# Kernel tuning notes

Measured on AMD Instinct MI355X. Metric: run time of the kernel, lower is better.

The kernel has to match this reference:

```python
import jax, jax.numpy as jnp
import numpy as np

DIM = 512
HEADS = 8


def setup_inputs() -> dict:
    key = jax.random.key(0)
    k1, k2, k3 = jax.random.split(key, 3)
    x = jax.random.normal(k1, (4, DIM, 64, 64), dtype=jnp.float32)
    # kaiming_normal fan_out, linear: std = 1/sqrt(fan_out)
    w_qkv = jax.random.normal(k2, (3 * DIM, DIM), dtype=jnp.float32) / np.sqrt(3 * DIM)
    b_qkv = jnp.zeros((3 * DIM,), dtype=jnp.float32)
    w_proj = jax.random.normal(k3, (DIM, DIM), dtype=jnp.float32) / np.sqrt(DIM)
    b_proj = jnp.zeros((DIM,), dtype=jnp.float32)
    return {"x": x, "w_qkv": w_qkv, "b_qkv": b_qkv, "w_proj": w_proj, "b_proj": b_proj}


def reference(x, w_qkv, b_qkv, w_proj, b_proj):
    B, C, H, W = x.shape
    N = H * W
    hd = C // HEADS
    scale = hd ** -0.5
    x_flat = x.reshape(B, C, N).transpose(0, 2, 1)          # [B, N, C]
    qkv = x_flat @ w_qkv.T + b_qkv                           # [B, N, 3C]
    q, k, v = jnp.split(qkv, 3, axis=-1)
    q = q.reshape(B, N, HEADS, hd).transpose(0, 2, 1, 3)     # [B, h, N, d]
    k = k.reshape(B, N, HEADS, hd).transpose(0, 2, 1, 3)
    v = v.reshape(B, N, HEADS, hd).transpose(0, 2, 1, 3)
    attn = jnp.einsum('bhnd,bhmd->bhnm', q, k) * scale       # [B, h, N, N]
    attn = jnp.clip(attn, -10.0, 10.0)
    attn = jax.nn.softmax(attn, axis=-1)
    out = jnp.einsum('bhnm,bhmd->bhnd', attn, v)             # [B, h, N, d]
    out = out.transpose(0, 2, 1, 3).reshape(B, N, C)         # [B, N, C]
    out = out @ w_proj.T + b_proj
    out = out.transpose(0, 2, 1).reshape(B, C, H, W)
    return x + out
```

## Files before the change

### kernel.cpp

```cpp
#include <hip/hip_runtime.h>

typedef float f32x4 __attribute__((ext_vector_type(4)));
typedef __bf16 bf16x8 __attribute__((ext_vector_type(8)));
typedef unsigned short u16;
typedef unsigned int u32;
typedef u16 u16x4 __attribute__((ext_vector_type(4)));
typedef u16 u16x8 __attribute__((ext_vector_type(8)));

#define DEV static __device__ __forceinline__

constexpr int B = 4, C = 512, NH = 8, HD = 64, NN = 4096, C3 = 1536;
constexpr float K_PRESCALE = 0.125f * 1.4426950408889634f;
constexpr float CLIP2 = 10.0f * 1.4426950408889634f;

DEV u16 f2bf(float f) { union { __bf16 b; u16 s; } u; u.b = (__bf16)f; return u.s; }

#if __has_builtin(__builtin_amdgcn_exp2f)
DEV float fast_exp2(float x) { return __builtin_amdgcn_exp2f(x); }
#else
DEV float fast_exp2(float x) { return __expf(x * 0.6931471805599453f); }
#endif

#if __has_builtin(__builtin_amdgcn_fmed3f)
DEV float clamp2(float x) { return __builtin_amdgcn_fmed3f(x, -CLIP2, CLIP2); }
#else
DEV float clamp2(float x) { return fminf(fmaxf(x, -CLIP2), CLIP2); }
#endif

__global__ __launch_bounds__(256) void k_transpose(const float* __restrict__ x,
                                                   u16* __restrict__ Xt) {
  __shared__ float tile[64][65];
  const int n0 = blockIdx.x * 64, c0 = blockIdx.y * 64, b = blockIdx.z;
  const int t = threadIdx.x;
  const int cl = t >> 4, n4 = (t & 15) * 4;
#pragma unroll
  for (int rep = 0; rep < 4; ++rep) {
    const int c = rep * 16 + cl;
    const f32x4 v = *(const f32x4*)(x + ((size_t)(b * C + c0 + c)) * NN + n0 + n4);
#pragma unroll
    for (int j = 0; j < 4; ++j) tile[c][n4 + j] = v[j];
  }
  __syncthreads();
#pragma unroll
  for (int rep = 0; rep < 16; ++rep) {
    const int n = rep * 4 + (t >> 6);
    const int c = t & 63;
    Xt[((size_t)(b * NN + n0 + n)) * C + c0 + c] = f2bf(tile[c][n]);
  }
}

__global__ __launch_bounds__(256) void k_cvtw(const float* __restrict__ wq,
                                              const float* __restrict__ wp,
                                              u16* __restrict__ Wq, u16* __restrict__ Wp) {
  const int idx = blockIdx.x * 256 + threadIdx.x;
  const int NQ = C3 * C / 4;
  const float* src;
  u16* dst;
  int i4;
  if (idx < NQ) { src = wq; dst = Wq; i4 = idx; }
  else          { src = wp; dst = Wp; i4 = idx - NQ; }
  const f32x4 v = *(const f32x4*)(src + (size_t)i4 * 4);
  u16x4 o;
#pragma unroll
  for (int j = 0; j < 4; ++j) o[j] = f2bf(v[j]);
  *(u16x4*)(dst + (size_t)i4 * 4) = o;
}

__global__ __launch_bounds__(256) void k_qkv(const u16* __restrict__ Xt,
                                             const u16* __restrict__ W,
                                             const float* __restrict__ bias,
                                             u16* __restrict__ Q, u16* __restrict__ Kq,
                                             u16* __restrict__ Vt) {
  __shared__ u16 smem[16384];
  u16* Alds = smem;
  u16* Blds = smem + 8192;
  const int nt = blockIdx.x, mt = blockIdx.y, b = blockIdx.z;
  const int t = threadIdx.x, w = t >> 6, l = t & 63;
  const int l15 = l & 15, l4 = l >> 4;
  const int wr = w >> 1, wc = w & 1;
  f32x4 acc[4][4] = {};
  const u16* Abase = Xt + (size_t)(b * NN + nt * 128) * C;
  const u16* Bbase = W + (size_t)(mt * 128) * C;

  for (int kt = 0; kt < C / 64; ++kt) {
    __syncthreads();
#pragma unroll
    for (int i = 0; i < 4; ++i) {
      const int cch = t + 256 * i;
      const int r = cch >> 3, kb = (cch & 7) * 16;
      const int sw = kb ^ ((r & 7) << 4);
      *(f32x4*)((char*)Alds + r * 128 + sw) =
          *(const f32x4*)((const char*)(Abase + (size_t)r * C + kt * 64) + kb);
      *(f32x4*)((char*)Blds + r * 128 + sw) =
          *(const f32x4*)((const char*)(Bbase + (size_t)r * C + kt * 64) + kb);
    }
    __syncthreads();
#pragma unroll
    for (int ks = 0; ks < 2; ++ks) {
      bf16x8 af[4], bfr[4];
#pragma unroll
      for (int ri = 0; ri < 4; ++ri) {
        const int row = wr * 64 + ri * 16 + l15;
        af[ri] = *(const bf16x8*)((const char*)Alds + row * 128 +
                                  ((ks * 64 + l4 * 16) ^ ((row & 7) << 4)));
      }
#pragma unroll
      for (int cj = 0; cj < 4; ++cj) {
        const int row = wc * 64 + cj * 16 + l15;
        bfr[cj] = *(const bf16x8*)((const char*)Blds + row * 128 +
                                   ((ks * 64 + l4 * 16) ^ ((row & 7) << 4)));
      }
#pragma unroll
      for (int ri = 0; ri < 4; ++ri)
#pragma unroll
        for (int cj = 0; cj < 4; ++cj)
          acc[ri][cj] = __builtin_amdgcn_mfma_f32_16x16x32_bf16(af[ri], bfr[cj], acc[ri][cj], 0, 0, 0);
    }
  }

  __syncthreads();
  const int sec = mt >> 2;
  const int mtl = mt & 3;
  if (sec < 2) {
#pragma unroll
    for (int ri = 0; ri < 4; ++ri)
#pragma unroll
      for (int cj = 0; cj < 4; ++cj) {
        const int m_l = wc * 64 + cj * 16 + l15;
        const float bv = bias[mt * 128 + m_l];
        const float sc = (sec == 1) ? K_PRESCALE : 1.0f;
#pragma unroll
        for (int r = 0; r < 4; ++r) {
          const int n_l = wr * 64 + ri * 16 + l4 * 4 + r;
          *(u16*)((char*)smem + n_l * 256 + ((m_l * 2) ^ ((n_l & 7) << 4))) =
              f2bf((acc[ri][cj][r] + bv) * sc);
        }
      }
    __syncthreads();
    u16* dst = (sec == 0) ? Q : Kq;
#pragma unroll
    for (int rep = 0; rep < 8; ++rep) {
      const int idx = rep * 256 + t;
      const int n_l = idx >> 4, ch = idx & 15;
      const u16x8 v = *(const u16x8*)((char*)smem + n_l * 256 + ((ch * 16) ^ ((n_l & 7) << 4)));
      const int hh = mtl * 2 + (ch >> 3), dd = (ch & 7) * 8;
      *(u16x8*)(dst + ((size_t)(b * NH + hh) * NN + nt * 128 + n_l) * HD + dd) = v;
    }
  } else {
#pragma unroll
    for (int ri = 0; ri < 4; ++ri)
#pragma unroll
      for (int cj = 0; cj < 4; ++cj) {
        const int m_l = wc * 64 + cj * 16 + l15;
        const float bv = bias[mt * 128 + m_l];
        const int nb = wr * 64 + ri * 16 + l4 * 4;
        u16x4 pv;
#pragma unroll
        for (int r = 0; r < 4; ++r) pv[r] = f2bf(acc[ri][cj][r] + bv);
        *(u16x4*)((char*)smem + m_l * 256 + ((nb * 2) ^ ((m_l & 7) << 4))) = pv;
      }
    __syncthreads();
#pragma unroll
    for (int rep = 0; rep < 8; ++rep) {
      const int idx = rep * 256 + t;
      const int m_l = idx >> 4, ch = idx & 15;
      const u16x8 v = *(const u16x8*)((char*)smem + m_l * 256 + ((ch * 16) ^ ((m_l & 7) << 4)));
      const int hh = mtl * 2 + (m_l >> 6), dd = m_l & 63;
      *(u16x8*)(Vt + ((size_t)(b * NH + hh) * HD + dd) * NN + nt * 128 + ch * 8) = v;
    }
  }
}

__global__ __launch_bounds__(256) void k_attn(const u16* __restrict__ Q,
                                              const u16* __restrict__ K,
                                              const u16* __restrict__ Vt,
                                              u16* __restrict__ AO) {
  __shared__ u16 Klds[2][4096];
  __shared__ u16 Vlds[2][4096];
  __shared__ u16 Plds[4096];
  const int qt = blockIdx.x, h = blockIdx.y, b = blockIdx.z;
  const int bh = b * NH + h;
  const int t = threadIdx.x, w = t >> 6, l = t & 63;
  const int l15 = l & 15, l4 = l >> 4;
  const int q0 = qt * 64;

  const u16* qb = Q + ((size_t)bh * NN + q0 + w * 16 + l15) * HD + l4 * 8;
  bf16x8 qf[2];
  qf[0] = *(const bf16x8*)(qb);
  qf[1] = *(const bf16x8*)(qb + 32);

  union { u16 s; __bf16 b; } ob;
  ob.s = 0x3F80;
  bf16x8 ones;
#pragma unroll
  for (int j = 0; j < 8; ++j) ones[j] = ob.b;

  f32x4 o[4] = {};
  f32x4 rsa = {};

  const int sr = t >> 3, scb = (t & 7) * 16;
  const int swoff = (scb ^ ((sr & 7) << 4)) + sr * 128;
  const char* kg = (const char*)(K + (size_t)bh * NN * HD) + sr * 128 + scb;
  const char* vg = (const char*)(Vt + (size_t)bh * HD * NN) + (size_t)sr * 8192 + scb;

  const int sw7 = (l15 & 7) << 4;

  {
    const f32x4 a0 = *(const f32x4*)kg;
    const f32x4 a1 = *(const f32x4*)(kg + 4096);
    const f32x4 a2 = *(const f32x4*)vg;
    const f32x4 a3 = *(const f32x4*)(vg + (size_t)32 * 8192);
    *(f32x4*)((char*)Klds + swoff) = a0;
    *(f32x4*)((char*)Klds + swoff + 4096) = a1;
    *(f32x4*)((char*)Vlds + swoff) = a2;
    *(f32x4*)((char*)Vlds + swoff + 4096) = a3;
  }
  __syncthreads();

  constexpr int NT = NN / 64;
  f32x4 kr0, kr1, vr0, vr1;
  for (int kv = 0; kv < NT; ++kv) {
    const int cur = kv & 1;
    const bool more = (kv + 1 < NT);
    if (more) {
      kg += 8192;
      vg += 128;
      kr0 = *(const f32x4*)kg;
      kr1 = *(const f32x4*)(kg + 4096);
      vr0 = *(const f32x4*)vg;
      vr1 = *(const f32x4*)(vg + (size_t)32 * 8192);
    }
    const char* kbase = (const char*)Klds + cur * 8192;
    const char* vbase = (const char*)Vlds + cur * 8192;

    f32x4 s[4] = {};
#pragma unroll
    for (int ks = 0; ks < 2; ++ks) {
#pragma unroll
      for (int cj = 0; cj < 4; ++cj) {
        const bf16x8 kf = *(const bf16x8*)(kbase + (cj * 16 + l15) * 128 +
                                           ((ks * 64 + l4 * 16) ^ sw7));
        s[cj] = __builtin_amdgcn_mfma_f32_16x16x32_bf16(qf[ks], kf, s[cj], 0, 0, 0);
      }
    }
#pragma unroll
    for (int cj = 0; cj < 4; ++cj) {
      const int colb = (cj * 16 + l15) * 2;
#pragma unroll
      for (int r = 0; r < 4; ++r) {
        const float p = fast_exp2(clamp2(s[cj][r]));
        const int row = w * 16 + l4 * 4 + r;
        *(u16*)((char*)Plds + row * 128 + (colb ^ ((row & 7) << 4))) = f2bf(p);
      }
    }

#pragma unroll
    for (int ks = 0; ks < 2; ++ks) {
      const int prow = w * 16 + l15;
      const bf16x8 pa = *(const bf16x8*)((const char*)Plds + prow * 128 +
                                         ((ks * 64 + l4 * 16) ^ sw7));
#pragma unroll
      for (int cj = 0; cj < 4; ++cj) {
        const bf16x8 vf = *(const bf16x8*)(vbase + (cj * 16 + l15) * 128 +
                                           ((ks * 64 + l4 * 16) ^ sw7));
        o[cj] = __builtin_amdgcn_mfma_f32_16x16x32_bf16(pa, vf, o[cj], 0, 0, 0);
      }
      rsa = __builtin_amdgcn_mfma_f32_16x16x32_bf16(pa, ones, rsa, 0, 0, 0);
    }

    if (more) {
      char* kw = (char*)Klds + (cur ^ 1) * 8192 + swoff;
      char* vw = (char*)Vlds + (cur ^ 1) * 8192 + swoff;
      *(f32x4*)kw = kr0;
      *(f32x4*)(kw + 4096) = kr1;
      *(f32x4*)vw = vr0;
      *(f32x4*)(vw + 4096) = vr1;
    }
    __syncthreads();
  }

  float inv[4];
#pragma unroll
  for (int r = 0; r < 4; ++r) inv[r] = 1.0f / rsa[r];
#pragma unroll
  for (int cj = 0; cj < 4; ++cj)
#pragma unroll
    for (int r = 0; r < 4; ++r) {
      const int n = q0 + w * 16 + l4 * 4 + r;
      const int c = h * 64 + cj * 16 + l15;
      AO[((size_t)(b * NN + n)) * C + c] = f2bf(o[cj][r] * inv[r]);
    }
}

__global__ __launch_bounds__(256) void k_proj(const u16* __restrict__ AO,
                                              const u16* __restrict__ Wp,
                                              const float* __restrict__ bias,
                                              const float* __restrict__ x,
                                              float* __restrict__ out) {
  __shared__ u16 smem[16384];
  u16* Alds = smem;
  u16* Blds = smem + 8192;
  const int nt = blockIdx.x, ct = blockIdx.y, b = blockIdx.z;
  const int t = threadIdx.x, w = t >> 6, l = t & 63;
  const int l15 = l & 15, l4 = l >> 4;
  const int wr = w >> 1, wc = w & 1;
  f32x4 acc[4][4] = {};
  const u16* Abase = AO + (size_t)(b * NN + nt * 128) * C;
  const u16* Bbase = Wp + (size_t)(ct * 128) * C;

  for (int kt = 0; kt < C / 64; ++kt) {
    __syncthreads();
#pragma unroll
    for (int i = 0; i < 4; ++i) {
      const int cch = t + 256 * i;
      const int r = cch >> 3, kb = (cch & 7) * 16;
      const int sw = kb ^ ((r & 7) << 4);
      *(f32x4*)((char*)Alds + r * 128 + sw) =
          *(const f32x4*)((const char*)(Abase + (size_t)r * C + kt * 64) + kb);
      *(f32x4*)((char*)Blds + r * 128 + sw) =
          *(const f32x4*)((const char*)(Bbase + (size_t)r * C + kt * 64) + kb);
    }
    __syncthreads();
#pragma unroll
    for (int ks = 0; ks < 2; ++ks) {
      bf16x8 af[4], bfr[4];
#pragma unroll
      for (int ri = 0; ri < 4; ++ri) {
        const int row = wr * 64 + ri * 16 + l15;
        af[ri] = *(const bf16x8*)((const char*)Alds + row * 128 +
                                  ((ks * 64 + l4 * 16) ^ ((row & 7) << 4)));
      }
#pragma unroll
      for (int cj = 0; cj < 4; ++cj) {
        const int row = wc * 64 + cj * 16 + l15;
        bfr[cj] = *(const bf16x8*)((const char*)Blds + row * 128 +
                                   ((ks * 64 + l4 * 16) ^ ((row & 7) << 4)));
      }
#pragma unroll
      for (int ri = 0; ri < 4; ++ri)
#pragma unroll
        for (int cj = 0; cj < 4; ++cj)
          acc[ri][cj] = __builtin_amdgcn_mfma_f32_16x16x32_bf16(af[ri], bfr[cj], acc[ri][cj], 0, 0, 0);
    }
  }

  float* fs = (float*)smem;
  __syncthreads();
#pragma unroll
  for (int p = 0; p < 2; ++p) {
    if (p) __syncthreads();
    if (wc == p) {
#pragma unroll
      for (int ri = 0; ri < 4; ++ri)
#pragma unroll
        for (int cj = 0; cj < 4; ++cj) {
          const int co = cj * 16 + l15;
          const float bv = bias[ct * 128 + p * 64 + co];
          const int nb = wr * 64 + ri * 16 + l4 * 4;
          f32x4 vv;
#pragma unroll
          for (int r = 0; r < 4; ++r) vv[r] = acc[ri][cj][r] + bv;
          *(f32x4*)((char*)fs + co * 512 + ((nb * 4) ^ ((co & 7) << 4))) = vv;
        }
    }
    __syncthreads();
#pragma unroll
    for (int rep = 0; rep < 8; ++rep) {
      const int idx = rep * 256 + t;
      const int co = idx >> 5, ch = idx & 31;
      f32x4 vv = *(const f32x4*)((char*)fs + co * 512 + ((ch * 16) ^ ((co & 7) << 4)));
      const size_t base = ((size_t)(b * C + ct * 128 + p * 64 + co)) * NN + nt * 128 + ch * 4;
      const f32x4 xr = *(const f32x4*)(x + base);
#pragma unroll
      for (int r = 0; r < 4; ++r) vv[r] += xr[r];
      *(f32x4*)(out + base) = vv;
    }
  }
}

extern "C" void kernel_launch(void* const* d_in, const int* in_sizes, int n_in,
                              void* d_out, int out_size, void* d_ws, size_t ws_size,
                              hipStream_t stream) {
  const float* x      = (const float*)d_in[0];
  const float* w_qkv  = (const float*)d_in[1];
  const float* b_qkv  = (const float*)d_in[2];
  const float* w_proj = (const float*)d_in[3];
  const float* b_proj = (const float*)d_in[4];
  float* out = (float*)d_out;
  char* ws = (char*)d_ws;

  const size_t SZ_XT = (size_t)B * NN * C * 2;
  const size_t SZ_WQ = (size_t)C3 * C * 2;
  const size_t SZ_WP = (size_t)C * C * 2;
  const size_t SZ_QK = (size_t)B * NH * NN * HD * 2;

  u16* Xt = (u16*)(ws);
  u16* Wq = (u16*)(ws + SZ_XT);
  u16* Wp = (u16*)(ws + SZ_XT + SZ_WQ);
  u16* Qb = (u16*)(ws + SZ_XT + SZ_WQ + SZ_WP);
  u16* Kb = (u16*)(ws + SZ_XT + SZ_WQ + SZ_WP + SZ_QK);
  u16* Vt = (u16*)(ws + SZ_XT + SZ_WQ + SZ_WP + 2 * SZ_QK);
  u16* AO = Xt;

  k_transpose<<<dim3(NN / 64, C / 64, B), 256, 0, stream>>>(x, Xt);
  k_cvtw<<<dim3((C3 * C + C * C) / 4 / 256), 256, 0, stream>>>(w_qkv, w_proj, Wq, Wp);
  k_qkv<<<dim3(NN / 128, C3 / 128, B), 256, 0, stream>>>(Xt, Wq, b_qkv, Qb, Kb, Vt);
  k_attn<<<dim3(NN / 64, NH, B), 256, 0, stream>>>(Qb, Kb, Vt, AO);
  k_proj<<<dim3(NN / 128, C / 128, B), 256, 0, stream>>>(AO, Wp, b_proj, x, out);
}
```

Measured before the change: 385.2 us.

## Keep softmax probabilities in registers via transposed QK MFMA and lane shuffles

Swaps the operands of the QK^T MFMA so each lane's score fragment is already laid out along the key dimension. The probabilities are then repacked into the PV MFMA A-operand with cross-lane shuffles instead of a round trip through an LDS P buffer. The row sum is accumulated in scalar registers and reduced with shuffles at the end, which replaces the extra ones-MFMA. This removes LDS writes and reads and frees LDS, in exchange for 8 shuffles per tile plus some select logic.

```diff
diff --git a/kernel.cpp b/kernel.cpp
--- a/kernel.cpp
+++ b/kernel.cpp
@@ -6,6 +6,7 @@
 typedef unsigned int u32;
 typedef u16 u16x4 __attribute__((ext_vector_type(4)));
 typedef u16 u16x8 __attribute__((ext_vector_type(8)));
+typedef u32 u32x4 __attribute__((ext_vector_type(4)));
 
 #define DEV static __device__ __forceinline__
 
@@ -177,7 +178,6 @@
                                               u16* __restrict__ AO) {
   __shared__ u16 Klds[2][4096];
   __shared__ u16 Vlds[2][4096];
-  __shared__ u16 Plds[4096];
   const int qt = blockIdx.x, h = blockIdx.y, b = blockIdx.z;
   const int bh = b * NH + h;
   const int t = threadIdx.x, w = t >> 6, l = t & 63;
@@ -189,14 +189,8 @@
   qf[0] = *(const bf16x8*)(qb);
   qf[1] = *(const bf16x8*)(qb + 32);
 
-  union { u16 s; __bf16 b; } ob;
-  ob.s = 0x3F80;
-  bf16x8 ones;
-#pragma unroll
-  for (int j = 0; j < 8; ++j) ones[j] = ob.b;
-
   f32x4 o[4] = {};
-  f32x4 rsa = {};
+  float rs = 0.f;
 
   const int sr = t >> 3, scb = (t & 7) * 16;
   const int swoff = (scb ^ ((sr & 7) << 4)) + sr * 128;
@@ -204,6 +198,10 @@
   const char* vg = (const char*)(Vt + (size_t)bh * HD * NN) + (size_t)sr * 8192 + scb;
 
   const int sw7 = (l15 & 7) << 4;
+
+  const int addr_a = ((l & 16) << 1) + l15;
+  const int addr_b = addr_a + 16;
+  const bool sel_hi = (l & 32) != 0;
 
   {
     const f32x4 a0 = *(const f32x4*)kg;
@@ -240,32 +238,43 @@
       for (int cj = 0; cj < 4; ++cj) {
         const bf16x8 kf = *(const bf16x8*)(kbase + (cj * 16 + l15) * 128 +
                                            ((ks * 64 + l4 * 16) ^ sw7));
-        s[cj] = __builtin_amdgcn_mfma_f32_16x16x32_bf16(qf[ks], kf, s[cj], 0, 0, 0);
-      }
-    }
+        s[cj] = __builtin_amdgcn_mfma_f32_16x16x32_bf16(kf, qf[ks], s[cj], 0, 0, 0);
+      }
+    }
+
+    u32 w32v[8];
 #pragma unroll
     for (int cj = 0; cj < 4; ++cj) {
-      const int colb = (cj * 16 + l15) * 2;
-#pragma unroll
-      for (int r = 0; r < 4; ++r) {
-        const float p = fast_exp2(clamp2(s[cj][r]));
-        const int row = w * 16 + l4 * 4 + r;
-        *(u16*)((char*)Plds + row * 128 + (colb ^ ((row & 7) << 4))) = f2bf(p);
-      }
-    }
-
+      const float p0 = fast_exp2(clamp2(s[cj][0]));
+      const float p1 = fast_exp2(clamp2(s[cj][1]));
+      const float p2 = fast_exp2(clamp2(s[cj][2]));
+      const float p3 = fast_exp2(clamp2(s[cj][3]));
+      rs += (p0 + p1) + (p2 + p3);
+      w32v[cj * 2 + 0] = (u32)f2bf(p0) | ((u32)f2bf(p1) << 16);
+      w32v[cj * 2 + 1] = (u32)f2bf(p2) | ((u32)f2bf(p3) << 16);
+    }
+
+    u32x4 pa32[2];
 #pragma unroll
     for (int ks = 0; ks < 2; ++ks) {
-      const int prow = w * 16 + l15;
-      const bf16x8 pa = *(const bf16x8*)((const char*)Plds + prow * 128 +
-                                         ((ks * 64 + l4 * 16) ^ sw7));
+      const u32 wh0 = sel_hi ? w32v[ks * 4 + 2] : w32v[ks * 4 + 0];
+      const u32 wh1 = sel_hi ? w32v[ks * 4 + 3] : w32v[ks * 4 + 1];
+      pa32[ks][0] = (u32)__shfl((int)wh0, addr_a, 64);
+      pa32[ks][1] = (u32)__shfl((int)wh1, addr_a, 64);
+      pa32[ks][2] = (u32)__shfl((int)wh0, addr_b, 64);
+      pa32[ks][3] = (u32)__shfl((int)wh1, addr_b, 64);
+    }
+
+#pragma unroll
+    for (int ks = 0; ks < 2; ++ks) {
+      union { u32x4 u; bf16x8 h; } pa;
+      pa.u = pa32[ks];
 #pragma unroll
       for (int cj = 0; cj < 4; ++cj) {
         const bf16x8 vf = *(const bf16x8*)(vbase + (cj * 16 + l15) * 128 +
                                            ((ks * 64 + l4 * 16) ^ sw7));
-        o[cj] = __builtin_amdgcn_mfma_f32_16x16x32_bf16(pa, vf, o[cj], 0, 0, 0);
-      }
-      rsa = __builtin_amdgcn_mfma_f32_16x16x32_bf16(pa, ones, rsa, 0, 0, 0);
+        o[cj] = __builtin_amdgcn_mfma_f32_16x16x32_bf16(pa.h, vf, o[cj], 0, 0, 0);
+      }
     }
 
     if (more) {
@@ -279,9 +288,13 @@
     __syncthreads();
   }
 
+  float v = rs;
+  v += __shfl_xor(v, 16, 64);
+  v += __shfl_xor(v, 32, 64);
   float inv[4];
 #pragma unroll
-  for (int r = 0; r < 4; ++r) inv[r] = 1.0f / rsa[r];
+  for (int r = 0; r < 4; ++r)
+    inv[r] = 1.0f / __shfl(v, (l & 48) | (((l >> 4) & 3) * 4 + r), 64);
 #pragma unroll
   for (int cj = 0; cj < 4; ++cj)
 #pragma unroll
```

After: 395.7 us. 1.03x slower.
